# Kernel optimization log

Hardware: AMD Instinct MI355X
Metric: run time of the kernel (lower is better)

Reference implementation:

```python
import jax, jax.numpy as jnp
import numpy as np

NEG_RATIO = 5          # neg_sample_ratio, also k (num_nodes-1 >> ratio)
THRESH = 0.7           # hard_neg_threshold
SMOOTH = 0.1           # label_smoothing
NUM_NODES = 200_000
DIM = 128
B = 1024               # batch size, all labels == 1 (all positives)
FILL_VAL = -1.0e9


def _l2_normalize(x, eps=1e-12):
    # F.normalize(p=2, dim=-1): divide by clamped L2 norm
    n = jnp.sqrt(jnp.sum(x * x, axis=-1, keepdims=True))
    return x / jnp.maximum(n, eps)


def setup_inputs() -> dict:
    key = jax.random.key(0)
    k1, k2, k3, k4 = jax.random.split(key, 4)
    src_nodes = jax.random.randint(k1, (B,), 0, NUM_NODES)
    dst_nodes = jax.random.randint(k2, (B,), 0, NUM_NODES)
    labels = jnp.ones((B,), dtype=jnp.float32)  # all positives -> pos_mask all True
    timestamps = jax.random.uniform(k3, (B,), dtype=jnp.float32)
    memory = jax.random.normal(k4, (NUM_NODES, DIM), dtype=jnp.float32)
    return {
        "src_nodes": src_nodes,
        "dst_nodes": dst_nodes,
        "labels": labels,
        "timestamps": timestamps,
        "memory": memory,
    }


def reference(src_nodes, dst_nodes, labels, timestamps, memory):
    # --- embedding gather + L2 normalize ---
    src_emb = memory[src_nodes]                      # [B, D]
    s = _l2_normalize(src_emb).astype(jnp.float16)   # use_half_precision=True
    c = _l2_normalize(memory).astype(jnp.float16)    # [N, D]

    # --- similarity [B, N], back to fp32 ---
    sim = jnp.matmul(s, c.T).astype(jnp.float32)

    # --- mask out ground-truth dst and below-threshold sims ---
    cols = jnp.arange(NUM_NODES)
    allowed = cols[None, :] != dst_nodes[:, None]    # exclude GT positives
    valid = allowed & (sim > THRESH)
    score = jnp.where(valid, sim, FILL_VAL)

    # --- top-k hard negatives per positive ---
    k = NEG_RATIO  # min(neg_sample_ratio, num_nodes-1)
    topk_vals, topk_idx = jax.lax.top_k(score, k)    # [B, k]
    is_real = (topk_vals > FILL_VAL + 1.0).reshape(-1)  # [B*k]

    # --- fallback random negatives (fixed-shape equivalent of the torch
    #     pack-real-then-pad-random assembly; total count == B*k either way) ---
    rkey = jax.random.key(42)
    rand_dst = jax.random.randint(rkey, (B * k,), 0, NUM_NODES)
    src_rep = jnp.repeat(src_nodes, k)               # [B*k]
    rand_dst = jnp.where(rand_dst == src_rep, (rand_dst + 1) % NUM_NODES, rand_dst)

    final_src = src_rep
    final_dst = jnp.where(is_real, topk_idx.reshape(-1), rand_dst)
    neg_ts = jnp.repeat(timestamps, k)

    # --- assemble augmented batch ---
    new_src = jnp.concatenate([src_nodes, final_src])
    new_dst = jnp.concatenate([dst_nodes, final_dst])
    new_labels = jnp.concatenate([labels, jnp.zeros((B * k,), labels.dtype)])
    new_ts = jnp.concatenate([timestamps, neg_ts])

    # --- label smoothing ---
    new_labels = new_labels * (1.0 - SMOOTH) + (1.0 - new_labels) * SMOOTH

    return new_src, new_dst, new_labels, new_ts, topk_vals
```

## Files before the change

kernel.cpp:

```cpp
#include <hip/hip_runtime.h>

#define NUM_NODES 200000
#define DIM 128
#define BATCH 1024
#define K_NEG 5
#define CAP 16
#define BN 256
#define THRESH 0.7f
#define FILL (-1.0e9f)

typedef __attribute__((ext_vector_type(8))) short short8;
typedef __attribute__((ext_vector_type(16))) float f32x16;

__device__ __forceinline__ unsigned short f2bf(float x) {
  unsigned u = __builtin_bit_cast(unsigned, x);
  return (unsigned short)((u + 0x7fffu + ((u >> 16) & 1u)) >> 16);
}

__device__ __forceinline__ void tf2x32(unsigned k0, unsigned k1,
                                       unsigned x0, unsigned x1,
                                       unsigned* o0, unsigned* o1) {
  unsigned ks2 = k0 ^ k1 ^ 0x1BD11BDAu;
  unsigned v0 = x0 + k0, v1 = x1 + k1;
#define TFR(r) { v0 += v1; v1 = (v1 << r) | (v1 >> (32 - r)); v1 ^= v0; }
  TFR(13) TFR(15) TFR(26) TFR(6)   v0 += k1;  v1 += ks2 + 1u;
  TFR(17) TFR(29) TFR(16) TFR(24)  v0 += ks2; v1 += k0 + 2u;
  TFR(13) TFR(15) TFR(26) TFR(6)   v0 += k0;  v1 += k1 + 3u;
  TFR(17) TFR(29) TFR(16) TFR(24)  v0 += k1;  v1 += ks2 + 4u;
  TFR(13) TFR(15) TFR(26) TFR(6)   v0 += ks2; v1 += k0 + 5u;
#undef TFR
  *o0 = v0; *o1 = v1;
}

__device__ __forceinline__ unsigned rbits32(unsigned ka, unsigned kb, unsigned m) {
  unsigned o0, o1;
  tf2x32(ka, kb, 0u, m, &o0, &o1);
  return o0 ^ o1;
}

__global__ void prep_kernel(const float* __restrict__ memory,
                            const int* __restrict__ src_nodes,
                            unsigned short* __restrict__ s16f,
                            int* __restrict__ cand_cnt) {
  int tid = threadIdx.x;
  int gid = blockIdx.x * 256 + tid;
  if (gid < BATCH) cand_cnt[gid] = 0;
  int row = blockIdx.x * 4 + (tid >> 6);
  int L = tid & 63;
  int s = src_nodes[row];
  float2 v = ((const float2*)(memory + (size_t)s * DIM))[L];
  float ss = v.x * v.x + v.y * v.y;
#pragma unroll
  for (int off = 32; off > 0; off >>= 1) ss += __shfl_xor(ss, off);
  float inv = 1.0f / fmaxf(sqrtf(ss), 1e-12f);
  unsigned p = (unsigned)f2bf(v.x * inv) | ((unsigned)f2bf(v.y * inv) << 16);
  int ms = row >> 5, l32 = row & 31;
  int c = L >> 2;
  int ks = c >> 1, half = c & 1;
  ((unsigned*)s16f)[(((ms * 8 + ks) * 64) + half * 32 + l32) * 4 + (L & 3)] = p;
}

__global__ __launch_bounds__(256, 2) void sim_scan_kernel(
    const float* __restrict__ memory,
    const unsigned short* __restrict__ s16f,
    const int* __restrict__ dst_nodes,
    int* __restrict__ cand_cnt,
    float* __restrict__ cand_val,
    int* __restrict__ cand_idx) {
  int tid = threadIdx.x;
  int wid = tid >> 6;
  int lane = tid & 63;
  int half = lane >> 5;
  int l32 = lane & 31;
  int jb = blockIdx.x * BN + wid * 64;

  short8 bf0[8], bf1[8];
#pragma unroll
  for (int js = 0; js < 2; ++js) {
    int j = jb + js * 32 + l32;
    bool jv = (j < NUM_NODES);
    const float4* rp4 = (const float4*)(memory + (size_t)j * DIM);
    float4 q[16];
#pragma unroll
    for (int ks = 0; ks < 8; ++ks) {
      q[ks * 2]     = jv ? rp4[ks * 4 + half * 2]     : make_float4(0.f, 0.f, 0.f, 0.f);
      q[ks * 2 + 1] = jv ? rp4[ks * 4 + half * 2 + 1] : make_float4(0.f, 0.f, 0.f, 0.f);
    }
    float ss = 0.0f;
#pragma unroll
    for (int i = 0; i < 16; ++i)
      ss += q[i].x * q[i].x + q[i].y * q[i].y + q[i].z * q[i].z + q[i].w * q[i].w;
    ss += __shfl_xor(ss, 32);
    float inv = 1.0f / fmaxf(sqrtf(ss), 1e-12f);
#pragma unroll
    for (int ks = 0; ks < 8; ++ks) {
      float4 a = q[ks * 2], b = q[ks * 2 + 1];
      short8 f;
      f[0] = (short)f2bf(a.x * inv); f[1] = (short)f2bf(a.y * inv);
      f[2] = (short)f2bf(a.z * inv); f[3] = (short)f2bf(a.w * inv);
      f[4] = (short)f2bf(b.x * inv); f[5] = (short)f2bf(b.y * inv);
      f[6] = (short)f2bf(b.z * inv); f[7] = (short)f2bf(b.w * inv);
      if (js == 0) bf0[ks] = f; else bf1[ks] = f;
    }
  }

  const short8* __restrict__ af = (const short8*)s16f;
  short8 acur[8], anext[8];
#pragma unroll
  for (int ks = 0; ks < 8; ++ks) acur[ks] = af[ks * 64 + lane];

  for (int ms = 0; ms < 32; ++ms) {
    if (ms < 31) {
#pragma unroll
      for (int ks = 0; ks < 8; ++ks) anext[ks] = af[((ms + 1) * 8 + ks) * 64 + lane];
    }
    f32x16 acc0, acc1;
#pragma unroll
    for (int i = 0; i < 16; ++i) { acc0[i] = 0.0f; acc1[i] = 0.0f; }
#pragma unroll
    for (int ks = 0; ks < 8; ++ks) {
      acc0 = __builtin_amdgcn_mfma_f32_32x32x16_bf16(acur[ks], bf0[ks], acc0, 0, 0, 0);
      acc1 = __builtin_amdgcn_mfma_f32_32x32x16_bf16(acur[ks], bf1[ks], acc1, 0, 0, 0);
    }
    float vm = acc0[0];
#pragma unroll
    for (int i = 1; i < 16; ++i) vm = fmaxf(vm, acc0[i]);
#pragma unroll
    for (int i = 0; i < 16; ++i) vm = fmaxf(vm, acc1[i]);
    if (vm > THRESH) {
#pragma unroll
      for (int js = 0; js < 2; ++js) {
        int gj = jb + js * 32 + l32;
#pragma unroll
        for (int r = 0; r < 16; ++r) {
          float v = (js == 0) ? acc0[r] : acc1[r];
          if (v > THRESH) {
            int gi = ms * 32 + (r & 3) + 8 * (r >> 2) + 4 * half;
            if (gj < NUM_NODES && gj != dst_nodes[gi]) {
              int p = atomicAdd(&cand_cnt[gi], 1);
              if (p < CAP) {
                cand_val[gi * CAP + p] = v;
                cand_idx[gi * CAP + p] = gj;
              }
            }
          }
        }
      }
    }
#pragma unroll
    for (int ks = 0; ks < 8; ++ks) acur[ks] = anext[ks];
  }
}

__global__ void finalize_kernel(const int* __restrict__ src_nodes,
                                const int* __restrict__ dst_nodes,
                                const float* __restrict__ labels,
                                const float* __restrict__ ts,
                                const int* __restrict__ cand_cnt,
                                const float* __restrict__ cand_val,
                                const int* __restrict__ cand_idx,
                                float* __restrict__ out) {
  int r = blockIdx.x * 256 + threadIdx.x;
  if (r >= BATCH) return;
  const int TOT = BATCH + BATCH * K_NEG;
  int srcv = src_nodes[r];
  float tsv = ts[r];
  out[r] = (float)srcv;
  out[TOT + r] = (float)dst_nodes[r];
  float l = labels[r];
  out[2 * TOT + r] = l * 0.9f + (1.0f - l) * 0.1f;
  out[3 * TOT + r] = tsv;

  int cnt = cand_cnt[r];
  cnt = cnt < CAP ? cnt : CAP;
  float cv[CAP]; int ci[CAP];
  for (int i = 0; i < cnt; ++i) { cv[i] = cand_val[r * CAP + i]; ci[i] = cand_idx[r * CAP + i]; }

  unsigned k1a, k1b, k2a, k2b;
  tf2x32(0u, 42u, 0u, 0u, &k1a, &k1b);
  tf2x32(0u, 42u, 0u, 1u, &k2a, &k2b);

  const unsigned span = 200000u;
  const unsigned mult = 167296u;

  for (int s = 0; s < K_NEG; ++s) {
    int sel = -1;
    for (int i = 0; i < cnt; ++i)
      if (sel < 0 || cv[i] > cv[sel] || (cv[i] == cv[sel] && ci[i] < ci[sel])) sel = i;
    float v = FILL; int idx = 0;
    if (sel >= 0) { v = cv[sel]; idx = ci[sel]; cv[sel] = FILL; ci[sel] = 0x7fffffff; }
    bool is_real = v > (FILL + 1.0f);

    unsigned m = (unsigned)(r * K_NEG + s);
    unsigned hi = rbits32(k1a, k1b, m);
    unsigned lo = rbits32(k2a, k2b, m);
    unsigned off = ((hi % span) * mult + (lo % span)) % span;
    int rd = (int)off;
    if (rd == srcv) rd = (rd + 1) % NUM_NODES;
    int fd = is_real ? idx : rd;

    int mi = (int)m;
    out[BATCH + mi] = (float)srcv;
    out[TOT + BATCH + mi] = (float)fd;
    out[2 * TOT + BATCH + mi] = 0.1f;
    out[3 * TOT + BATCH + mi] = tsv;
    out[4 * TOT + mi] = v;
  }
}

extern "C" void kernel_launch(void* const* d_in, const int* in_sizes, int n_in,
                              void* d_out, int out_size, void* d_ws, size_t ws_size,
                              hipStream_t stream) {
  const int* src = (const int*)d_in[0];
  const int* dst = (const int*)d_in[1];
  const float* labels = (const float*)d_in[2];
  const float* ts = (const float*)d_in[3];
  const float* memory = (const float*)d_in[4];
  float* out = (float*)d_out;

  char* ws = (char*)d_ws;
  unsigned short* s16f = (unsigned short*)ws;
  int* cand_cnt = (int*)(ws + 262144);
  float* cand_val = (float*)(ws + 266240);
  int* cand_idx = (int*)(ws + 331776);

  prep_kernel<<<256, 256, 0, stream>>>(memory, src, s16f, cand_cnt);
  int jblocks = (NUM_NODES + BN - 1) / BN;
  sim_scan_kernel<<<jblocks, 256, 0, stream>>>(memory, s16f, dst, cand_cnt, cand_val, cand_idx);
  finalize_kernel<<<(BATCH + 255) / 256, 256, 0, stream>>>(src, dst, labels, ts,
                                                           cand_cnt, cand_val, cand_idx, out);
}
```

Before: 209.0 us.

## Pre-normalize candidate rows into bf16 buffer and simplify scan loop

Adds a separate norm_kernel that L2-normalizes every memory row and writes it as bf16 into the workspace. The scan kernel then loads ready-made bf16 fragments instead of reading fp32 rows and normalizing them in place. It also drops the double-buffered A prefetch in favour of per-iteration loads, uses a tree max reduction, and raises launch bounds to 3 blocks per CU. The extra pass writes and rereads a 51 MB buffer, which may cost more than it saves since the original fused approach read the fp32 data only once.

```diff
diff --git a/kernel.cpp b/kernel.cpp
--- a/kernel.cpp
+++ b/kernel.cpp
@@ -8,6 +8,7 @@
 #define BN 256
 #define THRESH 0.7f
 #define FILL (-1.0e9f)
+#define NORM_BLOCKS 2048
 
 typedef __attribute__((ext_vector_type(8))) short short8;
 typedef __attribute__((ext_vector_type(16))) float f32x16;
@@ -38,6 +39,32 @@
   return o0 ^ o1;
 }
 
+__global__ void norm_kernel(const float* __restrict__ memory,
+                            unsigned short* __restrict__ cnorm) {
+  int gtid = blockIdx.x * 256 + threadIdx.x;
+  int wg = gtid >> 6;
+  int lane = threadIdx.x & 63;
+  int c = lane & 31;
+  int h = lane >> 5;
+  const int NW = NORM_BLOCKS * 4;
+#pragma unroll 2
+  for (int pair = wg; pair < NUM_NODES / 2; pair += NW) {
+    int row = pair * 2 + h;
+    const float4* rp = (const float4*)(memory + (size_t)row * DIM);
+    float4 v = rp[c];
+    float ss = v.x * v.x + v.y * v.y + v.z * v.z + v.w * v.w;
+    ss += __shfl_xor(ss, 1);
+    ss += __shfl_xor(ss, 2);
+    ss += __shfl_xor(ss, 4);
+    ss += __shfl_xor(ss, 8);
+    ss += __shfl_xor(ss, 16);
+    float inv = 1.0f / fmaxf(sqrtf(ss), 1e-12f);
+    unsigned p0 = (unsigned)f2bf(v.x * inv) | ((unsigned)f2bf(v.y * inv) << 16);
+    unsigned p1 = (unsigned)f2bf(v.z * inv) | ((unsigned)f2bf(v.w * inv) << 16);
+    ((uint2*)(cnorm + (size_t)row * DIM))[c] = make_uint2(p0, p1);
+  }
+}
+
 __global__ void prep_kernel(const float* __restrict__ memory,
                             const int* __restrict__ src_nodes,
                             unsigned short* __restrict__ s16f,
@@ -60,8 +87,10 @@
   ((unsigned*)s16f)[(((ms * 8 + ks) * 64) + half * 32 + l32) * 4 + (L & 3)] = p;
 }
 
-__global__ __launch_bounds__(256, 2) void sim_scan_kernel(
+template<bool USE_CNORM>
+__global__ __launch_bounds__(256, 3) void sim_scan_kernel(
     const float* __restrict__ memory,
+    const unsigned short* __restrict__ cnorm,
     const unsigned short* __restrict__ s16f,
     const int* __restrict__ dst_nodes,
     int* __restrict__ cand_cnt,
@@ -75,58 +104,74 @@
   int jb = blockIdx.x * BN + wid * 64;
 
   short8 bf0[8], bf1[8];
-#pragma unroll
-  for (int js = 0; js < 2; ++js) {
-    int j = jb + js * 32 + l32;
-    bool jv = (j < NUM_NODES);
-    const float4* rp4 = (const float4*)(memory + (size_t)j * DIM);
-    float4 q[16];
-#pragma unroll
-    for (int ks = 0; ks < 8; ++ks) {
-      q[ks * 2]     = jv ? rp4[ks * 4 + half * 2]     : make_float4(0.f, 0.f, 0.f, 0.f);
-      q[ks * 2 + 1] = jv ? rp4[ks * 4 + half * 2 + 1] : make_float4(0.f, 0.f, 0.f, 0.f);
-    }
-    float ss = 0.0f;
-#pragma unroll
-    for (int i = 0; i < 16; ++i)
-      ss += q[i].x * q[i].x + q[i].y * q[i].y + q[i].z * q[i].z + q[i].w * q[i].w;
-    ss += __shfl_xor(ss, 32);
-    float inv = 1.0f / fmaxf(sqrtf(ss), 1e-12f);
-#pragma unroll
-    for (int ks = 0; ks < 8; ++ks) {
-      float4 a = q[ks * 2], b = q[ks * 2 + 1];
-      short8 f;
-      f[0] = (short)f2bf(a.x * inv); f[1] = (short)f2bf(a.y * inv);
-      f[2] = (short)f2bf(a.z * inv); f[3] = (short)f2bf(a.w * inv);
-      f[4] = (short)f2bf(b.x * inv); f[5] = (short)f2bf(b.y * inv);
-      f[6] = (short)f2bf(b.z * inv); f[7] = (short)f2bf(b.w * inv);
-      if (js == 0) bf0[ks] = f; else bf1[ks] = f;
-    }
-  }
+  if constexpr (USE_CNORM) {
+#pragma unroll
+    for (int js = 0; js < 2; ++js) {
+      int j = jb + js * 32 + l32;
+      int jc = j < NUM_NODES ? j : (NUM_NODES - 1);
+      const short8* rp = (const short8*)(cnorm + (size_t)jc * DIM);
+#pragma unroll
+      for (int ks = 0; ks < 8; ++ks) {
+        short8 f = rp[ks * 2 + half];
+        if (js == 0) bf0[ks] = f; else bf1[ks] = f;
+      }
+    }
+  } else {
+#pragma unroll
+    for (int js = 0; js < 2; ++js) {
+      int j = jb + js * 32 + l32;
+      bool jv = (j < NUM_NODES);
+      const float4* rp4 = (const float4*)(memory + (size_t)j * DIM);
+      float4 q[16];
+#pragma unroll
+      for (int ks = 0; ks < 8; ++ks) {
+        q[ks * 2]     = jv ? rp4[ks * 4 + half * 2]     : make_float4(0.f, 0.f, 0.f, 0.f);
+        q[ks * 2 + 1] = jv ? rp4[ks * 4 + half * 2 + 1] : make_float4(0.f, 0.f, 0.f, 0.f);
+      }
+      float ss = 0.0f;
+#pragma unroll
+      for (int i = 0; i < 16; ++i)
+        ss += q[i].x * q[i].x + q[i].y * q[i].y + q[i].z * q[i].z + q[i].w * q[i].w;
+      ss += __shfl_xor(ss, 32);
+      float inv = 1.0f / fmaxf(sqrtf(ss), 1e-12f);
+#pragma unroll
+      for (int ks = 0; ks < 8; ++ks) {
+        float4 a = q[ks * 2], b = q[ks * 2 + 1];
+        short8 f;
+        f[0] = (short)f2bf(a.x * inv); f[1] = (short)f2bf(a.y * inv);
+        f[2] = (short)f2bf(a.z * inv); f[3] = (short)f2bf(a.w * inv);
+        f[4] = (short)f2bf(b.x * inv); f[5] = (short)f2bf(b.y * inv);
+        f[6] = (short)f2bf(b.z * inv); f[7] = (short)f2bf(b.w * inv);
+        if (js == 0) bf0[ks] = f; else bf1[ks] = f;
+      }
+    }
+  }
+
+  f32x16 Z;
+#pragma unroll
+  for (int i = 0; i < 16; ++i) Z[i] = 0.0f;
 
   const short8* __restrict__ af = (const short8*)s16f;
-  short8 acur[8], anext[8];
-#pragma unroll
-  for (int ks = 0; ks < 8; ++ks) acur[ks] = af[ks * 64 + lane];
 
   for (int ms = 0; ms < 32; ++ms) {
-    if (ms < 31) {
-#pragma unroll
-      for (int ks = 0; ks < 8; ++ks) anext[ks] = af[((ms + 1) * 8 + ks) * 64 + lane];
-    }
-    f32x16 acc0, acc1;
-#pragma unroll
-    for (int i = 0; i < 16; ++i) { acc0[i] = 0.0f; acc1[i] = 0.0f; }
-#pragma unroll
-    for (int ks = 0; ks < 8; ++ks) {
-      acc0 = __builtin_amdgcn_mfma_f32_32x32x16_bf16(acur[ks], bf0[ks], acc0, 0, 0, 0);
-      acc1 = __builtin_amdgcn_mfma_f32_32x32x16_bf16(acur[ks], bf1[ks], acc1, 0, 0, 0);
-    }
-    float vm = acc0[0];
-#pragma unroll
-    for (int i = 1; i < 16; ++i) vm = fmaxf(vm, acc0[i]);
-#pragma unroll
-    for (int i = 0; i < 16; ++i) vm = fmaxf(vm, acc1[i]);
+    short8 a[8];
+#pragma unroll
+    for (int ks = 0; ks < 8; ++ks) a[ks] = af[(ms * 8 + ks) * 64 + lane];
+    f32x16 acc0 = __builtin_amdgcn_mfma_f32_32x32x16_bf16(a[0], bf0[0], Z, 0, 0, 0);
+    f32x16 acc1 = __builtin_amdgcn_mfma_f32_32x32x16_bf16(a[0], bf1[0], Z, 0, 0, 0);
+#pragma unroll
+    for (int ks = 1; ks < 8; ++ks) {
+      acc0 = __builtin_amdgcn_mfma_f32_32x32x16_bf16(a[ks], bf0[ks], acc0, 0, 0, 0);
+      acc1 = __builtin_amdgcn_mfma_f32_32x32x16_bf16(a[ks], bf1[ks], acc1, 0, 0, 0);
+    }
+    float mx[16];
+#pragma unroll
+    for (int i = 0; i < 16; ++i) mx[i] = fmaxf(acc0[i], acc1[i]);
+#pragma unroll
+    for (int s = 8; s > 0; s >>= 1)
+#pragma unroll
+      for (int i = 0; i < s; ++i) mx[i] = fmaxf(mx[i], mx[i + s]);
+    float vm = mx[0];
     if (vm > THRESH) {
 #pragma unroll
       for (int js = 0; js < 2; ++js) {
@@ -147,8 +192,6 @@
         }
       }
     }
-#pragma unroll
-    for (int ks = 0; ks < 8; ++ks) acur[ks] = anext[ks];
   }
 }
 
@@ -219,14 +262,33 @@
   float* out = (float*)d_out;
 
   char* ws = (char*)d_ws;
-  unsigned short* s16f = (unsigned short*)ws;
-  int* cand_cnt = (int*)(ws + 262144);
-  float* cand_val = (float*)(ws + 266240);
-  int* cand_idx = (int*)(ws + 331776);
-
-  prep_kernel<<<256, 256, 0, stream>>>(memory, src, s16f, cand_cnt);
+  const size_t CN_BYTES = (size_t)NUM_NODES * DIM * 2;
+  const size_t NEED_BIG = CN_BYTES + 262144 + 4096 + 65536 + 65536;
   int jblocks = (NUM_NODES + BN - 1) / BN;
-  sim_scan_kernel<<<jblocks, 256, 0, stream>>>(memory, s16f, dst, cand_cnt, cand_val, cand_idx);
-  finalize_kernel<<<(BATCH + 255) / 256, 256, 0, stream>>>(src, dst, labels, ts,
-                                                           cand_cnt, cand_val, cand_idx, out);
-}
+
+  if (ws_size >= NEED_BIG) {
+    unsigned short* cnorm = (unsigned short*)ws;
+    unsigned short* s16f = (unsigned short*)(ws + CN_BYTES);
+    int* cand_cnt = (int*)(ws + CN_BYTES + 262144);
+    float* cand_val = (float*)(ws + CN_BYTES + 266240);
+    int* cand_idx = (int*)(ws + CN_BYTES + 331776);
+
+    norm_kernel<<<NORM_BLOCKS, 256, 0, stream>>>(memory, cnorm);
+    prep_kernel<<<256, 256, 0, stream>>>(memory, src, s16f, cand_cnt);
+    sim_scan_kernel<true><<<jblocks, 256, 0, stream>>>(memory, cnorm, s16f, dst,
+                                                       cand_cnt, cand_val, cand_idx);
+    finalize_kernel<<<(BATCH + 255) / 256, 256, 0, stream>>>(src, dst, labels, ts,
+                                                             cand_cnt, cand_val, cand_idx, out);
+  } else {
+    unsigned short* s16f = (unsigned short*)ws;
+    int* cand_cnt = (int*)(ws + 262144);
+    float* cand_val = (float*)(ws + 266240);
+    int* cand_idx = (int*)(ws + 331776);
+
+    prep_kernel<<<256, 256, 0, stream>>>(memory, src, s16f, cand_cnt);
+    sim_scan_kernel<false><<<jblocks, 256, 0, stream>>>(memory, (const unsigned short*)nullptr,
+                                                        s16f, dst, cand_cnt, cand_val, cand_idx);
+    finalize_kernel<<<(BATCH + 255) / 256, 256, 0, stream>>>(src, dst, labels, ts,
+                                                             cand_cnt, cand_val, cand_idx, out);
+  }
+}
```

After: 232.9 us. 1.11x slower.

## Stage query tiles through double-buffered LDS via global_load_lds, raise occupancy

Applied to the files above, without the earlier changes.

Query tiles (A operand) now go through a shared double-buffered LDS area using direct global-to-LDS loads, in place of per-wave register prefetch from global memory. Each block fetches a tile once instead of each wave fetching it. The candidate rows are re-read from global memory rather than kept in a 16-entry float4 array, and the launch-bounds occupancy target goes from 2 to 4. The max reduction becomes a tree. The cost is a block-wide barrier on every ms iteration and a second read of memory rows, which may hit in cache.

```diff
diff --git a/kernel.cpp b/kernel.cpp
--- a/kernel.cpp
+++ b/kernel.cpp
@@ -15,6 +15,13 @@
 __device__ __forceinline__ unsigned short f2bf(float x) {
   unsigned u = __builtin_bit_cast(unsigned, x);
   return (unsigned short)((u + 0x7fffu + ((u >> 16) & 1u)) >> 16);
+}
+
+__device__ __forceinline__ void stage16(const void* g, void* l) {
+  __builtin_amdgcn_global_load_lds(
+      (const __attribute__((address_space(1))) unsigned int*)g,
+      (__attribute__((address_space(3))) unsigned int*)l,
+      16, 0, 0);
 }
 
 __device__ __forceinline__ void tf2x32(unsigned k0, unsigned k1,
@@ -60,13 +67,15 @@
   ((unsigned*)s16f)[(((ms * 8 + ks) * 64) + half * 32 + l32) * 4 + (L & 3)] = p;
 }
 
-__global__ __launch_bounds__(256, 2) void sim_scan_kernel(
+__global__ __launch_bounds__(256, 4) void sim_scan_kernel(
     const float* __restrict__ memory,
     const unsigned short* __restrict__ s16f,
     const int* __restrict__ dst_nodes,
     int* __restrict__ cand_cnt,
     float* __restrict__ cand_val,
     int* __restrict__ cand_idx) {
+  __shared__ unsigned short abuf[2][4096];
+
   int tid = threadIdx.x;
   int wid = tid >> 6;
   int lane = tid & 63;
@@ -74,27 +83,34 @@
   int l32 = lane & 31;
   int jb = blockIdx.x * BN + wid * 64;
 
+  const char* s16b = (const char*)s16f;
+  {
+    const char* src = s16b + (wid << 10) + (lane << 4);
+    char* lb = (char*)&abuf[0][0] + (wid << 10);
+    stage16(src, lb);
+    stage16(src + 4096, lb + 4096);
+  }
+
   short8 bf0[8], bf1[8];
 #pragma unroll
   for (int js = 0; js < 2; ++js) {
     int j = jb + js * 32 + l32;
-    bool jv = (j < NUM_NODES);
-    const float4* rp4 = (const float4*)(memory + (size_t)j * DIM);
-    float4 q[16];
+    int jc = j < NUM_NODES ? j : (NUM_NODES - 1);
+    const float4* rp4 = (const float4*)(memory + (size_t)jc * DIM);
+    float ss = 0.0f;
 #pragma unroll
     for (int ks = 0; ks < 8; ++ks) {
-      q[ks * 2]     = jv ? rp4[ks * 4 + half * 2]     : make_float4(0.f, 0.f, 0.f, 0.f);
-      q[ks * 2 + 1] = jv ? rp4[ks * 4 + half * 2 + 1] : make_float4(0.f, 0.f, 0.f, 0.f);
-    }
-    float ss = 0.0f;
-#pragma unroll
-    for (int i = 0; i < 16; ++i)
-      ss += q[i].x * q[i].x + q[i].y * q[i].y + q[i].z * q[i].z + q[i].w * q[i].w;
+      float4 a = rp4[ks * 4 + half * 2];
+      float4 b = rp4[ks * 4 + half * 2 + 1];
+      ss += a.x * a.x + a.y * a.y + a.z * a.z + a.w * a.w;
+      ss += b.x * b.x + b.y * b.y + b.z * b.z + b.w * b.w;
+    }
     ss += __shfl_xor(ss, 32);
     float inv = 1.0f / fmaxf(sqrtf(ss), 1e-12f);
 #pragma unroll
     for (int ks = 0; ks < 8; ++ks) {
-      float4 a = q[ks * 2], b = q[ks * 2 + 1];
+      float4 a = rp4[ks * 4 + half * 2];
+      float4 b = rp4[ks * 4 + half * 2 + 1];
       short8 f;
       f[0] = (short)f2bf(a.x * inv); f[1] = (short)f2bf(a.y * inv);
       f[2] = (short)f2bf(a.z * inv); f[3] = (short)f2bf(a.w * inv);
@@ -104,30 +120,36 @@
     }
   }
 
-  const short8* __restrict__ af = (const short8*)s16f;
-  short8 acur[8], anext[8];
-#pragma unroll
-  for (int ks = 0; ks < 8; ++ks) acur[ks] = af[ks * 64 + lane];
+  __syncthreads();
+  int cur = 0;
 
   for (int ms = 0; ms < 32; ++ms) {
     if (ms < 31) {
-#pragma unroll
-      for (int ks = 0; ks < 8; ++ks) anext[ks] = af[((ms + 1) * 8 + ks) * 64 + lane];
-    }
+      const char* src = s16b + (size_t)(ms + 1) * 8192 + (wid << 10) + (lane << 4);
+      char* lb = (char*)&abuf[cur ^ 1][0] + (wid << 10);
+      stage16(src, lb);
+      stage16(src + 4096, lb + 4096);
+    }
+
+    const short8* ab = (const short8*)&abuf[cur][0];
     f32x16 acc0, acc1;
 #pragma unroll
     for (int i = 0; i < 16; ++i) { acc0[i] = 0.0f; acc1[i] = 0.0f; }
 #pragma unroll
     for (int ks = 0; ks < 8; ++ks) {
-      acc0 = __builtin_amdgcn_mfma_f32_32x32x16_bf16(acur[ks], bf0[ks], acc0, 0, 0, 0);
-      acc1 = __builtin_amdgcn_mfma_f32_32x32x16_bf16(acur[ks], bf1[ks], acc1, 0, 0, 0);
-    }
-    float vm = acc0[0];
-#pragma unroll
-    for (int i = 1; i < 16; ++i) vm = fmaxf(vm, acc0[i]);
-#pragma unroll
-    for (int i = 0; i < 16; ++i) vm = fmaxf(vm, acc1[i]);
-    if (vm > THRESH) {
+      short8 ak = ab[ks * 64 + lane];
+      acc0 = __builtin_amdgcn_mfma_f32_32x32x16_bf16(ak, bf0[ks], acc0, 0, 0, 0);
+      acc1 = __builtin_amdgcn_mfma_f32_32x32x16_bf16(ak, bf1[ks], acc1, 0, 0, 0);
+    }
+
+    float mx[16];
+#pragma unroll
+    for (int i = 0; i < 16; ++i) mx[i] = fmaxf(acc0[i], acc1[i]);
+#pragma unroll
+    for (int s = 8; s > 0; s >>= 1)
+#pragma unroll
+      for (int i = 0; i < s; ++i) mx[i] = fmaxf(mx[i], mx[i + s]);
+    if (mx[0] > THRESH) {
 #pragma unroll
       for (int js = 0; js < 2; ++js) {
         int gj = jb + js * 32 + l32;
@@ -147,8 +169,9 @@
         }
       }
     }
-#pragma unroll
-    for (int ks = 0; ks < 8; ++ks) acur[ks] = anext[ks];
+
+    __syncthreads();
+    cur ^= 1;
   }
 }
 
```

After: 233.5 us. +11.7%, slower.

## Defer candidate normalization to threshold and drop A-fragment prefetch to raise occupancy

Applied to the files above, without the earlier changes.

The candidate rows are now converted to bf16 unnormalized, and the per-column norm is folded into the threshold (raw > 0.7*norm), with the stored value rescaled by 1/norm only on a hit. The software double-buffer of A fragments is removed, a zero accumulator is reused, and launch bounds go from 2 to 4 blocks per SIMD, all to cut register pressure and allow more waves in flight. Out-of-range rows are clamped instead of zeroed. The trade-off is that bf16 rounding of raw values differs slightly from rounding normalized values, which can change near-threshold results. Losing the explicit prefetch may also expose load latency if the extra occupancy does not hide it.

```diff
diff --git a/kernel.cpp b/kernel.cpp
--- a/kernel.cpp
+++ b/kernel.cpp
@@ -60,7 +60,7 @@
   ((unsigned*)s16f)[(((ms * 8 + ks) * 64) + half * 32 + l32) * 4 + (L & 3)] = p;
 }
 
-__global__ __launch_bounds__(256, 2) void sim_scan_kernel(
+__global__ __launch_bounds__(256, 4) void sim_scan_kernel(
     const float* __restrict__ memory,
     const unsigned short* __restrict__ s16f,
     const int* __restrict__ dst_nodes,
@@ -75,71 +75,68 @@
   int jb = blockIdx.x * BN + wid * 64;
 
   short8 bf0[8], bf1[8];
+  float inv0, inv1, thr0, thr1;
 #pragma unroll
   for (int js = 0; js < 2; ++js) {
     int j = jb + js * 32 + l32;
-    bool jv = (j < NUM_NODES);
-    const float4* rp4 = (const float4*)(memory + (size_t)j * DIM);
-    float4 q[16];
+    int jc = j < NUM_NODES ? j : (NUM_NODES - 1);
+    const float4* rp4 = (const float4*)(memory + (size_t)jc * DIM);
+    float ss = 0.0f;
 #pragma unroll
     for (int ks = 0; ks < 8; ++ks) {
-      q[ks * 2]     = jv ? rp4[ks * 4 + half * 2]     : make_float4(0.f, 0.f, 0.f, 0.f);
-      q[ks * 2 + 1] = jv ? rp4[ks * 4 + half * 2 + 1] : make_float4(0.f, 0.f, 0.f, 0.f);
-    }
-    float ss = 0.0f;
-#pragma unroll
-    for (int i = 0; i < 16; ++i)
-      ss += q[i].x * q[i].x + q[i].y * q[i].y + q[i].z * q[i].z + q[i].w * q[i].w;
-    ss += __shfl_xor(ss, 32);
-    float inv = 1.0f / fmaxf(sqrtf(ss), 1e-12f);
-#pragma unroll
-    for (int ks = 0; ks < 8; ++ks) {
-      float4 a = q[ks * 2], b = q[ks * 2 + 1];
+      float4 a = rp4[ks * 4 + half * 2];
+      float4 b = rp4[ks * 4 + half * 2 + 1];
+      ss += a.x * a.x + a.y * a.y + a.z * a.z + a.w * a.w;
+      ss += b.x * b.x + b.y * b.y + b.z * b.z + b.w * b.w;
       short8 f;
-      f[0] = (short)f2bf(a.x * inv); f[1] = (short)f2bf(a.y * inv);
-      f[2] = (short)f2bf(a.z * inv); f[3] = (short)f2bf(a.w * inv);
-      f[4] = (short)f2bf(b.x * inv); f[5] = (short)f2bf(b.y * inv);
-      f[6] = (short)f2bf(b.z * inv); f[7] = (short)f2bf(b.w * inv);
+      f[0] = (short)f2bf(a.x); f[1] = (short)f2bf(a.y);
+      f[2] = (short)f2bf(a.z); f[3] = (short)f2bf(a.w);
+      f[4] = (short)f2bf(b.x); f[5] = (short)f2bf(b.y);
+      f[6] = (short)f2bf(b.z); f[7] = (short)f2bf(b.w);
       if (js == 0) bf0[ks] = f; else bf1[ks] = f;
     }
+    ss += __shfl_xor(ss, 32);
+    float nrm = fmaxf(sqrtf(ss), 1e-12f);
+    if (js == 0) { inv0 = 1.0f / nrm; thr0 = THRESH * nrm; }
+    else         { inv1 = 1.0f / nrm; thr1 = THRESH * nrm; }
   }
 
+  f32x16 Z;
+#pragma unroll
+  for (int i = 0; i < 16; ++i) Z[i] = 0.0f;
+
   const short8* __restrict__ af = (const short8*)s16f;
-  short8 acur[8], anext[8];
-#pragma unroll
-  for (int ks = 0; ks < 8; ++ks) acur[ks] = af[ks * 64 + lane];
 
   for (int ms = 0; ms < 32; ++ms) {
-    if (ms < 31) {
-#pragma unroll
-      for (int ks = 0; ks < 8; ++ks) anext[ks] = af[((ms + 1) * 8 + ks) * 64 + lane];
+    short8 a[8];
+#pragma unroll
+    for (int ks = 0; ks < 8; ++ks) a[ks] = af[(ms * 8 + ks) * 64 + lane];
+    f32x16 acc0 = __builtin_amdgcn_mfma_f32_32x32x16_bf16(a[0], bf0[0], Z, 0, 0, 0);
+    f32x16 acc1 = __builtin_amdgcn_mfma_f32_32x32x16_bf16(a[0], bf1[0], Z, 0, 0, 0);
+#pragma unroll
+    for (int ks = 1; ks < 8; ++ks) {
+      acc0 = __builtin_amdgcn_mfma_f32_32x32x16_bf16(a[ks], bf0[ks], acc0, 0, 0, 0);
+      acc1 = __builtin_amdgcn_mfma_f32_32x32x16_bf16(a[ks], bf1[ks], acc1, 0, 0, 0);
     }
-    f32x16 acc0, acc1;
-#pragma unroll
-    for (int i = 0; i < 16; ++i) { acc0[i] = 0.0f; acc1[i] = 0.0f; }
-#pragma unroll
-    for (int ks = 0; ks < 8; ++ks) {
-      acc0 = __builtin_amdgcn_mfma_f32_32x32x16_bf16(acur[ks], bf0[ks], acc0, 0, 0, 0);
-      acc1 = __builtin_amdgcn_mfma_f32_32x32x16_bf16(acur[ks], bf1[ks], acc1, 0, 0, 0);
-    }
-    float vm = acc0[0];
-#pragma unroll
-    for (int i = 1; i < 16; ++i) vm = fmaxf(vm, acc0[i]);
-#pragma unroll
-    for (int i = 0; i < 16; ++i) vm = fmaxf(vm, acc1[i]);
-    if (vm > THRESH) {
+
+    float m0 = acc0[0], m1 = acc1[0];
+#pragma unroll
+    for (int i = 1; i < 16; ++i) { m0 = fmaxf(m0, acc0[i]); m1 = fmaxf(m1, acc1[i]); }
+    if (m0 > thr0 || m1 > thr1) {
 #pragma unroll
       for (int js = 0; js < 2; ++js) {
         int gj = jb + js * 32 + l32;
+        float thr = (js == 0) ? thr0 : thr1;
+        float inv = (js == 0) ? inv0 : inv1;
 #pragma unroll
         for (int r = 0; r < 16; ++r) {
-          float v = (js == 0) ? acc0[r] : acc1[r];
-          if (v > THRESH) {
+          float raw = (js == 0) ? acc0[r] : acc1[r];
+          if (raw > thr) {
             int gi = ms * 32 + (r & 3) + 8 * (r >> 2) + 4 * half;
             if (gj < NUM_NODES && gj != dst_nodes[gi]) {
               int p = atomicAdd(&cand_cnt[gi], 1);
               if (p < CAP) {
-                cand_val[gi * CAP + p] = v;
+                cand_val[gi * CAP + p] = raw * inv;
                 cand_idx[gi * CAP + p] = gj;
               }
             }
@@ -147,8 +144,6 @@
         }
       }
     }
-#pragma unroll
-    for (int ks = 0; ks < 8; ++ks) acur[ks] = anext[ks];
   }
 }
 
```

Result: slower. 250.1 us (+19.6%).
